# Performance work log

Measured on AMD Instinct MI355X. Metric: run time of the kernel, lower is better.

The kernel has to match this reference:

```python
import jax, jax.numpy as jnp
import numpy as np
from jax import lax

DN = ('NDHWC', 'DHWIO', 'NDHWC')
EPS = 1e-4  # scn.BatchNormReLU default eps
B, D, H, W = 1, 41, 264, 264  # sparse_shape = grid_size[::-1] + [1,0,0]
N = 80000


def bn_relu(x, p):
    # p: (4, C) = [gamma, beta, running_mean, running_var]
    g, b, m, v = p[0], p[1], p[2], p[3]
    return jax.nn.relu((x - m) * (g * lax.rsqrt(v + EPS)) + b)


def subm_conv(x, mask, w, p):
    # submanifold conv: dense SAME conv, outputs only at active input sites
    y = lax.conv_general_dilated(x, w, (1, 1, 1), 'SAME', dimension_numbers=DN)
    return bn_relu(y, p) * mask


def sparse_conv(x, mask, w, p, stride, ksize):
    # scn.Convolution: VALID strided conv; output active where any input in RF is active
    y = lax.conv_general_dilated(x, w, stride, 'VALID', dimension_numbers=DN)
    m = lax.reduce_window(mask, 0.0, lax.max, (1,) + ksize + (1,), (1,) + stride + (1,), 'VALID')
    return bn_relu(y, p) * m, m


def setup_inputs() -> dict:
    key = jax.random.key(0)
    ks = jax.random.split(key, 32)

    voxel_features = jax.random.normal(ks[0], (N, 4), dtype=jnp.float32)
    bz = jnp.zeros((N,), jnp.int32)
    cz = jax.random.randint(ks[1], (N,), 0, D, dtype=jnp.int32)
    cy = jax.random.randint(ks[2], (N,), 0, H, dtype=jnp.int32)
    cx = jax.random.randint(ks[3], (N,), 0, W, dtype=jnp.int32)
    voxel_coords = jnp.stack([bz, cz, cy, cx], axis=1)

    def mk_w(k, shape):
        std = 1.0 / np.sqrt(float(np.prod(shape[:4])))
        return jax.random.normal(k, shape, dtype=jnp.float32) * std

    def mk_bn(k, c):
        k1, k2, k3, k4 = jax.random.split(k, 4)
        g = jax.random.uniform(k1, (c,), minval=0.5, maxval=1.5)
        b = jax.random.normal(k2, (c,)) * 0.1
        m = jax.random.normal(k3, (c,)) * 0.1
        v = jax.random.uniform(k4, (c,), minval=0.5, maxval=1.5)
        return jnp.stack([g, b, m, v]).astype(jnp.float32)

    inp = {'voxel_features': voxel_features, 'voxel_coords': voxel_coords}
    specs = [('1a', (3, 3, 3, 4, 16)), ('1b', (3, 3, 3, 16, 16)),
             ('2a', (3, 3, 3, 16, 32)), ('2b', (3, 3, 3, 32, 32)),
             ('3a', (3, 3, 3, 32, 64)), ('3b', (3, 3, 3, 64, 64)),
             ('4a', (3, 3, 3, 64, 64)), ('4b', (3, 3, 3, 64, 64)),
             ('out', (3, 1, 1, 64, 128))]
    for i, (tag, shp) in enumerate(specs):
        inp['w' + tag] = mk_w(ks[4 + 2 * i], shp)
        inp['bn' + tag] = mk_bn(ks[5 + 2 * i], shp[-1])
    return inp


def reference(voxel_features, voxel_coords, w1a, bn1a, w1b, bn1b, w2a, bn2a, w2b, bn2b,
              w3a, bn3a, w3b, bn3b, w4a, bn4a, w4b, bn4b, wout, bnout):
    b, z, y, x = voxel_coords[:, 0], voxel_coords[:, 1], voxel_coords[:, 2], voxel_coords[:, 3]
    dense = jnp.zeros((B, D, H, W, voxel_features.shape[-1]), voxel_features.dtype)
    dense = dense.at[b, z, y, x].set(voxel_features)
    mask = jnp.zeros((B, D, H, W, 1), voxel_features.dtype).at[b, z, y, x].set(1.0)

    x1 = subm_conv(dense, mask, w1a, bn1a)
    x1 = subm_conv(x1, mask, w1b, bn1b)

    x2, m2 = sparse_conv(x1, mask, w2a, bn2a, (2, 2, 2), (3, 3, 3))
    x2 = subm_conv(x2, m2, w2b, bn2b)

    x3, m3 = sparse_conv(x2, m2, w3a, bn3a, (2, 2, 2), (3, 3, 3))
    x3 = subm_conv(x3, m3, w3b, bn3b)

    x4, m4 = sparse_conv(x3, m3, w4a, bn4a, (2, 2, 2), (3, 3, 3))
    x4 = subm_conv(x4, m4, w4b, bn4b)

    out, _ = sparse_conv(x4, m4, wout, bnout, (1, 1, 1), (3, 1, 1))
    return out  # (1, 2, 32, 32, 128), stride-8 encoded sparse tensor (dense emulation)
```

## Files before the change

### kernel.cpp

```cpp
#include <hip/hip_runtime.h>

#define EPSV 1e-4f

typedef short bf16x8 __attribute__((ext_vector_type(8)));
typedef float f32x4 __attribute__((ext_vector_type(4)));

constexpr int D1=41, H1=264, W1=264; constexpr int S1=D1*H1*W1;
constexpr int D2=20, H2=131, W2=131; constexpr int S2=D2*H2*W2;
constexpr int D3=9,  H3=65,  W3=65;  constexpr int S3=D3*H3*W3;
constexpr int D4=4,  H4=32,  W4=32;  constexpr int S4=D4*H4*W4;
constexpr int DO_=2, HO_=32, WO_=32; constexpr int SO_=DO_*HO_*WO_;
constexpr int NVOX_MAX=80000;

__device__ __forceinline__ unsigned short bf_rne(float f){
  unsigned int x = __float_as_uint(f);
  unsigned int r = (x + 0x7FFFu + ((x>>16)&1u)) >> 16;
  return (unsigned short)r;
}
__device__ __forceinline__ float bf_tof(unsigned short u){
  return __uint_as_float(((unsigned int)u)<<16);
}

__global__ void scatter_k(const int* __restrict__ coords, int n, int* __restrict__ grid1){
  int i = blockIdx.x*blockDim.x + threadIdx.x;
  if (i >= n) return;
  int z = coords[i*4+1], y = coords[i*4+2], x = coords[i*4+3];
  atomicMax(&grid1[(z*H1 + y)*W1 + x], i);
}

__global__ void compact1_k(int* __restrict__ grid1, int* __restrict__ act,
                           int* __restrict__ vox, int* __restrict__ cnt){
  __shared__ int lcnt, lbase;
  if (threadIdx.x == 0) lcnt = 0;
  __syncthreads();
  int p = blockIdx.x*blockDim.x + threadIdx.x;
  int v = (p < S1) ? grid1[p] : -1;
  int loc = -1;
  if (v >= 0) loc = atomicAdd(&lcnt, 1);
  __syncthreads();
  if (threadIdx.x == 0) lbase = (lcnt > 0) ? atomicAdd(cnt, lcnt) : 0;
  __syncthreads();
  if (v >= 0){ int r = lbase + loc; act[r] = p; vox[r] = v; grid1[p] = r; }
}

__global__ void gather0_k(const float4* __restrict__ vf, const int* __restrict__ vox,
                          const int* __restrict__ cnt, float4* __restrict__ f0){
  int r = blockIdx.x*blockDim.x + threadIdx.x;
  if (r >= *cnt) return;
  f0[r] = vf[vox[r]];
}

#define FMA4(acc, f, w0, w1, w2, w3)                      \
  acc.x = fmaf(f.x, w0.x, acc.x); acc.y = fmaf(f.x, w0.y, acc.y); \
  acc.z = fmaf(f.x, w0.z, acc.z); acc.w = fmaf(f.x, w0.w, acc.w); \
  acc.x = fmaf(f.y, w1.x, acc.x); acc.y = fmaf(f.y, w1.y, acc.y); \
  acc.z = fmaf(f.y, w1.z, acc.z); acc.w = fmaf(f.y, w1.w, acc.w); \
  acc.x = fmaf(f.z, w2.x, acc.x); acc.y = fmaf(f.z, w2.y, acc.y); \
  acc.z = fmaf(f.z, w2.z, acc.z); acc.w = fmaf(f.z, w2.w, acc.w); \
  acc.x = fmaf(f.w, w3.x, acc.x); acc.y = fmaf(f.w, w3.y, acc.y); \
  acc.z = fmaf(f.w, w3.z, acc.z); acc.w = fmaf(f.w, w3.w, acc.w)

template<int CIN,int COUT,bool SUBM,int DI,int HI,int WI,int HOo,int WOo,
         int SD,int SH,int SW,bool HLOUT>
__global__ __launch_bounds__(256) void conv_sw_k(
    const float* __restrict__ fin, const float* __restrict__ w,
    const float* __restrict__ bnp, const int* __restrict__ grid,
    const int* __restrict__ act, const int* __restrict__ cnt,
    void* __restrict__ fout_v)
{
  constexpr int NT  = 27;
  constexpr int NCO = 8;
  constexpr int NCG = COUT/NCO;
  const int lane = threadIdx.x & 63;
  const int wgl  = blockIdx.x*4 + (threadIdx.x >> 6);
  const int sblk = wgl / NCG;
  const int cg   = wgl % NCG;
  int co = __builtin_amdgcn_readfirstlane(cg*NCO);
  const int n = *cnt;
  if (sblk*64 >= n) return;
  const int r = sblk*64 + lane;
  const bool ok = r < n;

  int z=0, y=0, x=0;
  if (ok){ int p = act[r]; x = p % WOo; int t1 = p/WOo; y = t1 % HOo; z = t1/HOo; }

  auto gidx = [&](int kk)->int {
    if (!ok) return -1;
    int kd = kk/9, kh = (kk/3)%3, kw2 = kk%3;
    if (SUBM){
      if (kk == 13) return r;
      int zz = z + kd - 1, yy = y + kh - 1, xx = x + kw2 - 1;
      if ((unsigned)zz >= (unsigned)DI || (unsigned)yy >= (unsigned)HI ||
          (unsigned)xx >= (unsigned)WI) return -1;
      return grid[(zz*HI + yy)*WI + xx];
    } else {
      int zz = z*SD + kd, yy = y*SH + kh, xx = x*SW + kw2;
      return grid[(zz*HI + yy)*WI + xx];
    }
  };

  float4 acc0 = {0.f,0.f,0.f,0.f}, acc1 = {0.f,0.f,0.f,0.f};
  int rr0 = gidx(0);
  int rr1 = gidx(1);
  #pragma unroll 1
  for (int kk = 0; kk < NT; kk++){
    int rrn = (kk + 2 < NT) ? gidx(kk+2) : -1;
    if (rr0 >= 0){
      const float4* fi = (const float4*)(fin + (size_t)rr0*CIN);
      const float* wt = w + (size_t)kk*CIN*COUT + co;
      #pragma unroll 8
      for (int c4 = 0; c4 < CIN/4; c4++){
        float4 f  = fi[c4];
        const float* wq = wt + c4*4*COUT;
        {
          float4 w0 = *(const float4*)(wq);
          float4 w1 = *(const float4*)(wq + COUT);
          float4 w2 = *(const float4*)(wq + 2*COUT);
          float4 w3 = *(const float4*)(wq + 3*COUT);
          FMA4(acc0, f, w0, w1, w2, w3);
        }
        {
          float4 w0 = *(const float4*)(wq + 4);
          float4 w1 = *(const float4*)(wq + COUT + 4);
          float4 w2 = *(const float4*)(wq + 2*COUT + 4);
          float4 w3 = *(const float4*)(wq + 3*COUT + 4);
          FMA4(acc1, f, w0, w1, w2, w3);
        }
      }
    }
    rr0 = rr1; rr1 = rrn;
  }
  if (ok){
    float o[8];
    float av[8] = {acc0.x,acc0.y,acc0.z,acc0.w, acc1.x,acc1.y,acc1.z,acc1.w};
    #pragma unroll
    for (int k = 0; k < 8; k++){
      int c = co + k;
      float g = bnp[c], b = bnp[COUT+c], m = bnp[2*COUT+c], v = bnp[3*COUT+c];
      o[k] = fmaxf((av[k] - m) * (g * rsqrtf(v + EPSV)) + b, 0.f);
    }
    if constexpr (HLOUT){
      unsigned short* fout = (unsigned short*)fout_v;
      bf16x8 vh, vl;
      #pragma unroll
      for (int k = 0; k < 8; k++){
        unsigned short hi = bf_rne(o[k]);
        vh[k] = (short)hi;
        vl[k] = (short)bf_rne(o[k] - bf_tof(hi));
      }
      *(bf16x8*)(fout + (size_t)r*2*COUT + co) = vh;
      *(bf16x8*)(fout + (size_t)r*2*COUT + COUT + co) = vl;
    } else {
      float* fout = (float*)fout_v;
      float4 o0 = {o[0],o[1],o[2],o[3]}, o1 = {o[4],o[5],o[6],o[7]};
      *(float4*)(fout + (size_t)r*COUT + co) = o0;
      *(float4*)(fout + (size_t)r*COUT + co + 4) = o1;
    }
  }
}

__global__ void wprep_k(const float* __restrict__ w, unsigned short* __restrict__ whi,
                        unsigned short* __restrict__ wlo, int CIN_, int COUT_, int NK_){
  int tid = blockIdx.x*256 + threadIdx.x;
  int total = NK_*COUT_*32;
  if (tid >= total) return;
  int j = tid & 7; int kgrp = (tid>>3)&3; int rest = tid>>5;
  int nn = rest % COUT_; int c = rest / COUT_;
  int kflat = c*32 + kgrp*8 + j;
  int tap = kflat / CIN_; int cin = kflat % CIN_;
  float val = w[((size_t)tap*CIN_ + cin)*COUT_ + nn];
  unsigned short hi = bf_rne(val);
  whi[tid] = hi;
  wlo[tid] = bf_rne(val - bf_tof(hi));
}

template<int CIN,int COUT,bool SUBM,int DI,int HI,int WI,int HOo,int WOo,
         int SD,int SH,int SW>
__global__ __launch_bounds__(256) void conv_mfma_k(
    const unsigned short* __restrict__ fin, const unsigned short* __restrict__ wBhi,
    const unsigned short* __restrict__ wBlo, const float* __restrict__ bnp,
    const int* __restrict__ grid, const int* __restrict__ act,
    const int* __restrict__ cnt, unsigned short* __restrict__ fout)
{
  constexpr int NK  = 27*CIN/32;
  constexpr int NTN = COUT/16;
  constexpr int MT  = NTN;
  constexpr int LDA = 40;
  __shared__ int act_lds[64];
  __shared__ int rr_lds[27*64];
  __shared__ unsigned short AhiL[2][64*LDA];
  __shared__ unsigned short AloL[2][64*LDA];

  const int tid  = threadIdx.x;
  const int lane = tid & 63;
  const int wv   = tid >> 6;
  const int blk  = blockIdx.x;
  const int n    = *cnt;
  if (blk*64 >= n) return;

  if (tid < 64){
    int r = blk*64 + tid;
    act_lds[tid] = (r < n) ? act[r] : -1;
  }
  __syncthreads();
  for (int idx = tid; idx < 27*64; idx += 256){
    int s = idx & 63, tap = idx >> 6;
    int p = act_lds[s];
    int rr = -1;
    if (p >= 0){
      int x = p % WOo; int t1 = p / WOo; int y = t1 % HOo; int z = t1 / HOo;
      int kd = tap/9, kh = (tap/3)%3, kw2 = tap%3;
      if (SUBM){
        if (tap == 13) rr = blk*64 + s;
        else {
          int zz = z+kd-1, yy = y+kh-1, xx = x+kw2-1;
          if ((unsigned)zz < (unsigned)DI && (unsigned)yy < (unsigned)HI &&
              (unsigned)xx < (unsigned)WI)
            rr = grid[(zz*HI+yy)*WI+xx];
        }
      } else {
        int zz = z*SD+kd, yy = y*SH+kh, xx = x*SW+kw2;
        rr = grid[(zz*HI+yy)*WI+xx];
      }
    }
    rr_lds[idx] = rr;
  }
  __syncthreads();

  const int ss = tid >> 2;
  const int sq = tid & 3;
  const bf16x8 zv = {0,0,0,0,0,0,0,0};

  auto stage_load = [&](int c, bf16x8& v0, bf16x8& v1){
    int tap = (c*32)/CIN;
    int ks  = (c*32)%CIN;
    int rr  = rr_lds[tap*64 + ss];
    if (rr >= 0){
      int eoff = (sq < 2) ? (ks + sq*16) : (CIN + ks + (sq-2)*16);
      const bf16x8* sp = (const bf16x8*)(fin + (size_t)rr*2*CIN + eoff);
      v0 = sp[0]; v1 = sp[1];
    } else { v0 = zv; v1 = zv; }
  };
  auto stage_write = [&](int b, bf16x8 v0, bf16x8 v1){
    unsigned short* base = (sq < 2) ? &AhiL[b][ss*LDA + sq*16]
                                    : &AloL[b][ss*LDA + (sq-2)*16];
    ((bf16x8*)base)[0] = v0; ((bf16x8*)base)[1] = v1;
  };

  const int nt    = wv % NTN;
  const int mbase = (wv / NTN) * MT;
  const int l15   = lane & 15;
  const int lg    = lane >> 4;

  f32x4 acc[MT];
  #pragma unroll
  for (int i = 0; i < MT; i++) acc[i] = (f32x4){0.f,0.f,0.f,0.f};

  {
    bf16x8 s0, s1;
    stage_load(0, s0, s1);
    stage_write(0, s0, s1);
  }
  __syncthreads();

  #pragma unroll 1
  for (int c = 0; c < NK; c++){
    const int b = c & 1;
    bf16x8 n0 = zv, n1 = zv;
    if (c + 1 < NK) stage_load(c+1, n0, n1);

    size_t bidx = ((size_t)(c*COUT + nt*16 + l15)*4 + lg) * 8;
    bf16x8 Bh = *(const bf16x8*)(wBhi + bidx);
    bf16x8 Bl = *(const bf16x8*)(wBlo + bidx);

    #pragma unroll
    for (int i = 0; i < MT; i++){
      int row = (mbase + i)*16 + l15;
      bf16x8 Ah = *(const bf16x8*)(&AhiL[b][row*LDA + lg*8]);
      bf16x8 Al = *(const bf16x8*)(&AloL[b][row*LDA + lg*8]);
      acc[i] = __builtin_amdgcn_mfma_f32_16x16x32_bf16(Ah, Bh, acc[i], 0, 0, 0);
      acc[i] = __builtin_amdgcn_mfma_f32_16x16x32_bf16(Ah, Bl, acc[i], 0, 0, 0);
      acc[i] = __builtin_amdgcn_mfma_f32_16x16x32_bf16(Al, Bh, acc[i], 0, 0, 0);
    }

    if (c + 1 < NK) stage_write(b ^ 1, n0, n1);
    __syncthreads();
  }

  const int cout = nt*16 + l15;
  const float g = bnp[cout], bb = bnp[COUT+cout];
  const float mm = bnp[2*COUT+cout], vv = bnp[3*COUT+cout];
  const float sc = g * rsqrtf(vv + EPSV);
  #pragma unroll
  for (int i = 0; i < MT; i++){
    #pragma unroll
    for (int reg = 0; reg < 4; reg++){
      int srow = (mbase + i)*16 + lg*4 + reg;
      int r = blk*64 + srow;
      if (r < n){
        float o = fmaxf((acc[i][reg] - mm) * sc + bb, 0.f);
        unsigned short hi = bf_rne(o);
        unsigned short lo = bf_rne(o - bf_tof(hi));
        fout[(size_t)r*2*COUT + cout] = hi;
        fout[(size_t)r*2*COUT + COUT + cout] = lo;
      }
    }
  }
}

template<int DI,int HI,int WI,int DDo,int HHo,int WWo,int KD,int KH,int KW,int SD,int SH,int SW>
__global__ void build_k(const int* __restrict__ gin, int* __restrict__ gout,
                        int* __restrict__ act, int* __restrict__ cnt){
  __shared__ int lcnt, lbase;
  if (threadIdx.x == 0) lcnt = 0;
  __syncthreads();
  int p = blockIdx.x*blockDim.x + threadIdx.x;
  bool any = false;
  if (p < DDo*HHo*WWo){
    int x = p % WWo; int rem = p / WWo; int y = rem % HHo; int z = rem / HHo;
    for (int kd = 0; kd < KD; kd++)
      for (int kh = 0; kh < KH; kh++)
        for (int kw = 0; kw < KW; kw++){
          if (gin[((z*SD+kd)*HI + (y*SH+kh))*WI + (x*SW+kw)] >= 0) any = true;
        }
  }
  int loc = -1;
  if (any) loc = atomicAdd(&lcnt, 1);
  __syncthreads();
  if (threadIdx.x == 0) lbase = (lcnt > 0) ? atomicAdd(cnt, lcnt) : 0;
  __syncthreads();
  if (p < DDo*HHo*WWo){
    int r = any ? (lbase + loc) : -1;
    if (any) act[r] = p;
    gout[p] = r;
  }
}

__global__ __launch_bounds__(256) void out_conv_k(
    const unsigned short* __restrict__ f4, const float* __restrict__ w,
    const float* __restrict__ bnp, const int* __restrict__ g4,
    float* __restrict__ out){
  int t = blockIdx.x*blockDim.x + threadIdx.x;
  if (t >= SO_*32) return;
  int co = (t % 32)*4; int p = t / 32;
  int x = p % WO_; int rem = p / WO_; int y = rem % HO_; int z = rem / HO_;
  bool any = false; float4 acc = {0.f,0.f,0.f,0.f};
  for (int kd = 0; kd < 3; kd++){
    int rr = g4[((z+kd)*H4 + y)*W4 + x];
    if (rr < 0) continue;
    any = true;
    const unsigned short* row = f4 + (size_t)rr*128;
    const float* wp = w + (size_t)kd*64*128 + co;
    #pragma unroll 4
    for (int ci = 0; ci < 64; ci++){
      float f = bf_tof(row[ci]) + bf_tof(row[64+ci]);
      const float* wq = wp + (size_t)ci*128;
      acc.x = fmaf(f, wq[0], acc.x); acc.y = fmaf(f, wq[1], acc.y);
      acc.z = fmaf(f, wq[2], acc.z); acc.w = fmaf(f, wq[3], acc.w);
    }
  }
  float4 o = {0.f,0.f,0.f,0.f};
  if (any){
    float4 g = *(const float4*)(bnp + co);
    float4 b = *(const float4*)(bnp + 128 + co);
    float4 m = *(const float4*)(bnp + 2*128 + co);
    float4 v = *(const float4*)(bnp + 3*128 + co);
    o.x = fmaxf((acc.x - m.x) * (g.x * rsqrtf(v.x + EPSV)) + b.x, 0.f);
    o.y = fmaxf((acc.y - m.y) * (g.y * rsqrtf(v.y + EPSV)) + b.y, 0.f);
    o.z = fmaxf((acc.z - m.z) * (g.z * rsqrtf(v.z + EPSV)) + b.z, 0.f);
    o.w = fmaxf((acc.w - m.w) * (g.w * rsqrtf(v.w + EPSV)) + b.w, 0.f);
  }
  *(float4*)(out + (size_t)p*128 + co) = o;
}

extern "C" void kernel_launch(void* const* d_in, const int* in_sizes, int n_in,
                              void* d_out, int out_size, void* d_ws, size_t ws_size,
                              hipStream_t stream){
  const float* vf  = (const float*)d_in[0];
  const int*   vc  = (const int*)  d_in[1];
  const float* w1a = (const float*)d_in[2];  const float* bn1a = (const float*)d_in[3];
  const float* w1b = (const float*)d_in[4];  const float* bn1b = (const float*)d_in[5];
  const float* w2a = (const float*)d_in[6];  const float* bn2a = (const float*)d_in[7];
  const float* w2b = (const float*)d_in[8];  const float* bn2b = (const float*)d_in[9];
  const float* w3a = (const float*)d_in[10]; const float* bn3a = (const float*)d_in[11];
  const float* w3b = (const float*)d_in[12]; const float* bn3b = (const float*)d_in[13];
  const float* w4a = (const float*)d_in[14]; const float* bn4a = (const float*)d_in[15];
  const float* w4b = (const float*)d_in[16]; const float* bn4b = (const float*)d_in[17];
  const float* wo  = (const float*)d_in[18]; const float* bno  = (const float*)d_in[19];
  float* outp = (float*)d_out;
  int nvox = in_sizes[0] / 4;
  if (nvox > NVOX_MAX) nvox = NVOX_MAX;

  char* ws = (char*)d_ws;
  size_t off = 0;
  auto alloc = [&](size_t bytes)->void*{
    void* p = ws + off; off = (off + bytes + 255) & ~size_t(255); return p;
  };
  int* grid1 = (int*)alloc((size_t)S1*4);
  int* act1  = (int*)alloc((size_t)NVOX_MAX*4);
  int* vox1  = (int*)alloc((size_t)NVOX_MAX*4);
  int* grid2 = (int*)alloc((size_t)S2*4);
  int* act2  = (int*)alloc((size_t)S2*4);
  int* grid3 = (int*)alloc((size_t)S3*4);
  int* act3  = (int*)alloc((size_t)S3*4);
  int* grid4 = (int*)alloc((size_t)S4*4);
  int* act4  = (int*)alloc((size_t)S4*4);
  int* cnt   = (int*)alloc(8*4);
  size_t f0_b  = (size_t)NVOX_MAX*4*4;
  size_t f1_b  = (size_t)NVOX_MAX*16*4;
  size_t f2_b  = (size_t)S2*64*2;
  size_t f3_b  = (size_t)S3*128*2;
  size_t f4_b  = (size_t)S4*128*2;
  float* f0  = (float*)alloc(f0_b);
  float* f1a = (float*)alloc(f1_b);
  float* f1b = (float*)alloc(f1_b);
  unsigned short* f2a = (unsigned short*)alloc(f2_b);
  unsigned short* f2b = (unsigned short*)alloc(f2_b);
  unsigned short* f3a = (unsigned short*)alloc(f3_b);
  unsigned short* f3b = (unsigned short*)alloc(f3_b);
  unsigned short* f4a = (unsigned short*)alloc(f4_b);
  unsigned short* f4b = (unsigned short*)alloc(f4_b);
  unsigned short* p2b_h = (unsigned short*)alloc((size_t)27*32*32*2);
  unsigned short* p2b_l = (unsigned short*)alloc((size_t)27*32*32*2);
  unsigned short* p3a_h = (unsigned short*)alloc((size_t)27*32*64*2);
  unsigned short* p3a_l = (unsigned short*)alloc((size_t)27*32*64*2);
  unsigned short* p3b_h = (unsigned short*)alloc((size_t)54*32*64*2);
  unsigned short* p3b_l = (unsigned short*)alloc((size_t)54*32*64*2);
  unsigned short* p4a_h = (unsigned short*)alloc((size_t)54*32*64*2);
  unsigned short* p4a_l = (unsigned short*)alloc((size_t)54*32*64*2);
  unsigned short* p4b_h = (unsigned short*)alloc((size_t)54*32*64*2);
  unsigned short* p4b_l = (unsigned short*)alloc((size_t)54*32*64*2);
  (void)ws_size;

  hipMemsetAsync(grid1, 0xFF, (size_t)S1*4, stream);
  hipMemsetAsync(cnt, 0, 8*4, stream);
  hipMemsetAsync(f0,  0, f0_b, stream);
  hipMemsetAsync(f1a, 0, f1_b, stream);
  hipMemsetAsync(f1b, 0, f1_b, stream);
  hipMemsetAsync(f2a, 0, f2_b, stream);
  hipMemsetAsync(f2b, 0, f2_b, stream);
  hipMemsetAsync(f3a, 0, f3_b, stream);
  hipMemsetAsync(f3b, 0, f3_b, stream);
  hipMemsetAsync(f4a, 0, f4_b, stream);
  hipMemsetAsync(f4b, 0, f4_b, stream);

  const int BS = 256;
  auto wprep = [&](const float* w, unsigned short* h, unsigned short* l, int cin, int cout, int nk){
    int total = nk*cout*32;
    wprep_k<<<(total+BS-1)/BS, BS, 0, stream>>>(w, h, l, cin, cout, nk);
  };
  wprep(w2b, p2b_h, p2b_l, 32, 32, 27);
  wprep(w3a, p3a_h, p3a_l, 32, 64, 27);
  wprep(w3b, p3b_h, p3b_l, 64, 64, 54);
  wprep(w4a, p4a_h, p4a_l, 64, 64, 54);
  wprep(w4b, p4b_h, p4b_l, 64, 64, 54);

  scatter_k<<<(nvox+BS-1)/BS, BS, 0, stream>>>(vc, nvox, grid1);
  compact1_k<<<(S1+BS-1)/BS, BS, 0, stream>>>(grid1, act1, vox1, &cnt[0]);
  gather0_k<<<(nvox+BS-1)/BS, BS, 0, stream>>>((const float4*)vf, vox1, &cnt[0], (float4*)f0);

  auto nblk = [](int maxN, int cout){ int waves = ((maxN+63)/64) * (cout/8); return (waves+3)/4; };

  conv_sw_k<4,16,true,D1,H1,W1,H1,W1,1,1,1,false>
    <<<nblk(NVOX_MAX,16), BS, 0, stream>>>(f0,  w1a, bn1a, grid1, act1, &cnt[0], f1a);
  conv_sw_k<16,16,true,D1,H1,W1,H1,W1,1,1,1,false>
    <<<nblk(NVOX_MAX,16), BS, 0, stream>>>(f1a, w1b, bn1b, grid1, act1, &cnt[0], f1b);

  build_k<D1,H1,W1,D2,H2,W2,3,3,3,2,2,2><<<(S2+BS-1)/BS, BS, 0, stream>>>(grid1, grid2, act2, &cnt[1]);
  conv_sw_k<16,32,false,D1,H1,W1,H2,W2,2,2,2,true>
    <<<nblk(S2,32), BS, 0, stream>>>(f1b, w2a, bn2a, grid1, act2, &cnt[1], f2a);
  conv_mfma_k<32,32,true,D2,H2,W2,H2,W2,1,1,1>
    <<<(S2+63)/64, BS, 0, stream>>>(f2a, p2b_h, p2b_l, bn2b, grid2, act2, &cnt[1], f2b);

  build_k<D2,H2,W2,D3,H3,W3,3,3,3,2,2,2><<<(S3+BS-1)/BS, BS, 0, stream>>>(grid2, grid3, act3, &cnt[2]);
  conv_mfma_k<32,64,false,D2,H2,W2,H3,W3,2,2,2>
    <<<(S3+63)/64, BS, 0, stream>>>(f2b, p3a_h, p3a_l, bn3a, grid2, act3, &cnt[2], f3a);
  conv_mfma_k<64,64,true,D3,H3,W3,H3,W3,1,1,1>
    <<<(S3+63)/64, BS, 0, stream>>>(f3a, p3b_h, p3b_l, bn3b, grid3, act3, &cnt[2], f3b);

  build_k<D3,H3,W3,D4,H4,W4,3,3,3,2,2,2><<<(S4+BS-1)/BS, BS, 0, stream>>>(grid3, grid4, act4, &cnt[3]);
  conv_mfma_k<64,64,false,D3,H3,W3,H4,W4,2,2,2>
    <<<(S4+63)/64, BS, 0, stream>>>(f3b, p4a_h, p4a_l, bn4a, grid3, act4, &cnt[3], f4a);
  conv_mfma_k<64,64,true,D4,H4,W4,H4,W4,1,1,1>
    <<<(S4+63)/64, BS, 0, stream>>>(f4a, p4b_h, p4b_l, bn4b, grid4, act4, &cnt[3], f4b);

  out_conv_k<<<(SO_*32+BS-1)/BS, BS, 0, stream>>>(f4b, wo, bno, grid4, outp);
}
```

Measured before the change: 687.6 us.

## Move conv1b and conv2a to split-bf16 MFMA and compact voxels directly

```diff
diff --git a/kernel.cpp b/kernel.cpp
--- a/kernel.cpp
+++ b/kernel.cpp
@@ -21,26 +21,25 @@
   return __uint_as_float(((unsigned int)u)<<16);
 }
 
-__global__ void scatter_k(const int* __restrict__ coords, int n, int* __restrict__ grid1){
+__global__ void scatter_k(const int* __restrict__ coords, int n, int* __restrict__ vgrid){
   int i = blockIdx.x*blockDim.x + threadIdx.x;
   if (i >= n) return;
   int z = coords[i*4+1], y = coords[i*4+2], x = coords[i*4+3];
-  atomicMax(&grid1[(z*H1 + y)*W1 + x], i);
-}
-
-__global__ void compact1_k(int* __restrict__ grid1, int* __restrict__ act,
-                           int* __restrict__ vox, int* __restrict__ cnt){
-  __shared__ int lcnt, lbase;
-  if (threadIdx.x == 0) lcnt = 0;
-  __syncthreads();
-  int p = blockIdx.x*blockDim.x + threadIdx.x;
-  int v = (p < S1) ? grid1[p] : -1;
-  int loc = -1;
-  if (v >= 0) loc = atomicAdd(&lcnt, 1);
-  __syncthreads();
-  if (threadIdx.x == 0) lbase = (lcnt > 0) ? atomicAdd(cnt, lcnt) : 0;
-  __syncthreads();
-  if (v >= 0){ int r = lbase + loc; act[r] = p; vox[r] = v; grid1[p] = r; }
+  atomicMax(&vgrid[(z*H1 + y)*W1 + x], i);
+}
+
+__global__ void compactv_k(const int* __restrict__ coords, int n,
+                           const int* __restrict__ vgrid, int* __restrict__ grid1,
+                           int* __restrict__ act, int* __restrict__ vox,
+                           int* __restrict__ cnt){
+  int i = blockIdx.x*blockDim.x + threadIdx.x;
+  if (i >= n) return;
+  int z = coords[i*4+1], y = coords[i*4+2], x = coords[i*4+3];
+  int p = (z*H1 + y)*W1 + x;
+  if (vgrid[p] == i){
+    int r = atomicAdd(cnt, 1);
+    act[r] = p; vox[r] = i; grid1[p] = r;
+  }
 }
 
 __global__ void gather0_k(const float4* __restrict__ vf, const int* __restrict__ vox,
@@ -167,6 +166,7 @@
   int j = tid & 7; int kgrp = (tid>>3)&3; int rest = tid>>5;
   int nn = rest % COUT_; int c = rest / COUT_;
   int kflat = c*32 + kgrp*8 + j;
+  if (kflat >= 27*CIN_){ whi[tid] = 0; wlo[tid] = 0; return; }
   int tap = kflat / CIN_; int cin = kflat % CIN_;
   float val = w[((size_t)tap*CIN_ + cin)*COUT_ + nn];
   unsigned short hi = bf_rne(val);
@@ -182,9 +182,9 @@
     const int* __restrict__ grid, const int* __restrict__ act,
     const int* __restrict__ cnt, unsigned short* __restrict__ fout)
 {
-  constexpr int NK  = 27*CIN/32;
+  constexpr int NK  = (27*CIN + 31)/32;
   constexpr int NTN = COUT/16;
-  constexpr int MT  = NTN;
+  constexpr int MT  = (NTN > 1) ? NTN : 1;
   constexpr int LDA = 40;
   __shared__ int act_lds[64];
   __shared__ int rr_lds[27*64];
@@ -232,18 +232,19 @@
   const bf16x8 zv = {0,0,0,0,0,0,0,0};
 
   auto stage_load = [&](int c, bf16x8& v0, bf16x8& v1){
-    int tap = (c*32)/CIN;
-    int ks  = (c*32)%CIN;
-    int rr  = rr_lds[tap*64 + ss];
+    int kseg = c*32 + (sq&1)*16;
+    int tap  = kseg / CIN;
+    int ch   = kseg % CIN;
+    int rr   = (tap < 27) ? rr_lds[tap*64 + ss] : -1;
     if (rr >= 0){
-      int eoff = (sq < 2) ? (ks + sq*16) : (CIN + ks + (sq-2)*16);
+      int eoff = (sq < 2) ? ch : (CIN + ch);
       const bf16x8* sp = (const bf16x8*)(fin + (size_t)rr*2*CIN + eoff);
       v0 = sp[0]; v1 = sp[1];
     } else { v0 = zv; v1 = zv; }
   };
   auto stage_write = [&](int b, bf16x8 v0, bf16x8 v1){
-    unsigned short* base = (sq < 2) ? &AhiL[b][ss*LDA + sq*16]
-                                    : &AloL[b][ss*LDA + (sq-2)*16];
+    unsigned short* base = (sq < 2) ? &AhiL[b][ss*LDA + (sq&1)*16]
+                                    : &AloL[b][ss*LDA + (sq&1)*16];
     ((bf16x8*)base)[0] = v0; ((bf16x8*)base)[1] = v1;
   };
 
@@ -396,6 +397,7 @@
   auto alloc = [&](size_t bytes)->void*{
     void* p = ws + off; off = (off + bytes + 255) & ~size_t(255); return p;
   };
+  int* vgrid = (int*)alloc((size_t)S1*4);
   int* grid1 = (int*)alloc((size_t)S1*4);
   int* act1  = (int*)alloc((size_t)NVOX_MAX*4);
   int* vox1  = (int*)alloc((size_t)NVOX_MAX*4);
@@ -407,19 +409,23 @@
   int* act4  = (int*)alloc((size_t)S4*4);
   int* cnt   = (int*)alloc(8*4);
   size_t f0_b  = (size_t)NVOX_MAX*4*4;
-  size_t f1_b  = (size_t)NVOX_MAX*16*4;
+  size_t f1_b  = (size_t)NVOX_MAX*32*2;
   size_t f2_b  = (size_t)S2*64*2;
   size_t f3_b  = (size_t)S3*128*2;
   size_t f4_b  = (size_t)S4*128*2;
   float* f0  = (float*)alloc(f0_b);
-  float* f1a = (float*)alloc(f1_b);
-  float* f1b = (float*)alloc(f1_b);
+  unsigned short* f1a = (unsigned short*)alloc(f1_b);
+  unsigned short* f1b = (unsigned short*)alloc(f1_b);
   unsigned short* f2a = (unsigned short*)alloc(f2_b);
   unsigned short* f2b = (unsigned short*)alloc(f2_b);
   unsigned short* f3a = (unsigned short*)alloc(f3_b);
   unsigned short* f3b = (unsigned short*)alloc(f3_b);
   unsigned short* f4a = (unsigned short*)alloc(f4_b);
   unsigned short* f4b = (unsigned short*)alloc(f4_b);
+  unsigned short* p1b_h = (unsigned short*)alloc((size_t)14*32*16*2);
+  unsigned short* p1b_l = (unsigned short*)alloc((size_t)14*32*16*2);
+  unsigned short* p2a_h = (unsigned short*)alloc((size_t)14*32*32*2);
+  unsigned short* p2a_l = (unsigned short*)alloc((size_t)14*32*32*2);
   unsigned short* p2b_h = (unsigned short*)alloc((size_t)27*32*32*2);
   unsigned short* p2b_l = (unsigned short*)alloc((size_t)27*32*32*2);
   unsigned short* p3a_h = (unsigned short*)alloc((size_t)27*32*64*2);
@@ -432,6 +438,7 @@
   unsigned short* p4b_l = (unsigned short*)alloc((size_t)54*32*64*2);
   (void)ws_size;
 
+  hipMemsetAsync(vgrid, 0xFF, (size_t)S1*4, stream);
   hipMemsetAsync(grid1, 0xFF, (size_t)S1*4, stream);
   hipMemsetAsync(cnt, 0, 8*4, stream);
   hipMemsetAsync(f0,  0, f0_b, stream);
@@ -449,26 +456,28 @@
     int total = nk*cout*32;
     wprep_k<<<(total+BS-1)/BS, BS, 0, stream>>>(w, h, l, cin, cout, nk);
   };
+  wprep(w1b, p1b_h, p1b_l, 16, 16, 14);
+  wprep(w2a, p2a_h, p2a_l, 16, 32, 14);
   wprep(w2b, p2b_h, p2b_l, 32, 32, 27);
   wprep(w3a, p3a_h, p3a_l, 32, 64, 27);
   wprep(w3b, p3b_h, p3b_l, 64, 64, 54);
   wprep(w4a, p4a_h, p4a_l, 64, 64, 54);
   wprep(w4b, p4b_h, p4b_l, 64, 64, 54);
 
-  scatter_k<<<(nvox+BS-1)/BS, BS, 0, stream>>>(vc, nvox, grid1);
-  compact1_k<<<(S1+BS-1)/BS, BS, 0, stream>>>(grid1, act1, vox1, &cnt[0]);
+  scatter_k<<<(nvox+BS-1)/BS, BS, 0, stream>>>(vc, nvox, vgrid);
+  compactv_k<<<(nvox+BS-1)/BS, BS, 0, stream>>>(vc, nvox, vgrid, grid1, act1, vox1, &cnt[0]);
   gather0_k<<<(nvox+BS-1)/BS, BS, 0, stream>>>((const float4*)vf, vox1, &cnt[0], (float4*)f0);
 
   auto nblk = [](int maxN, int cout){ int waves = ((maxN+63)/64) * (cout/8); return (waves+3)/4; };
 
-  conv_sw_k<4,16,true,D1,H1,W1,H1,W1,1,1,1,false>
-    <<<nblk(NVOX_MAX,16), BS, 0, stream>>>(f0,  w1a, bn1a, grid1, act1, &cnt[0], f1a);
-  conv_sw_k<16,16,true,D1,H1,W1,H1,W1,1,1,1,false>
-    <<<nblk(NVOX_MAX,16), BS, 0, stream>>>(f1a, w1b, bn1b, grid1, act1, &cnt[0], f1b);
+  conv_sw_k<4,16,true,D1,H1,W1,H1,W1,1,1,1,true>
+    <<<nblk(NVOX_MAX,16), BS, 0, stream>>>(f0, w1a, bn1a, grid1, act1, &cnt[0], f1a);
+  conv_mfma_k<16,16,true,D1,H1,W1,H1,W1,1,1,1>
+    <<<(NVOX_MAX+63)/64, BS, 0, stream>>>(f1a, p1b_h, p1b_l, bn1b, grid1, act1, &cnt[0], f1b);
 
   build_k<D1,H1,W1,D2,H2,W2,3,3,3,2,2,2><<<(S2+BS-1)/BS, BS, 0, stream>>>(grid1, grid2, act2, &cnt[1]);
-  conv_sw_k<16,32,false,D1,H1,W1,H2,W2,2,2,2,true>
-    <<<nblk(S2,32), BS, 0, stream>>>(f1b, w2a, bn2a, grid1, act2, &cnt[1], f2a);
+  conv_mfma_k<16,32,false,D1,H1,W1,H2,W2,2,2,2>
+    <<<(S2+63)/64, BS, 0, stream>>>(f1b, p2a_h, p2a_l, bn2a, grid1, act2, &cnt[1], f2a);
   conv_mfma_k<32,32,true,D2,H2,W2,H2,W2,1,1,1>
     <<<(S2+63)/64, BS, 0, stream>>>(f2a, p2b_h, p2b_l, bn2b, grid2, act2, &cnt[1], f2b);
 
```

Result: faster. 558.8 us (-18.7%).
